# Kernel optimization log

Hardware: AMD Instinct MI355X
Metric: run time of the kernel (lower is better)

The kernel has to match this reference:

```python
import jax, jax.numpy as jnp
import numpy as np

N_NODES = 100000
IN_DIM = 64
OUT_DIM = 64
N_EDGES = 1600000


def _undirected_self_loops(edge_index, num_nodes):
    """Symmetrize, add self loops, coalesce (dedup+sort) like the torch module.
    edge_index is an integer constant, so we preprocess with numpy (no grads flow here).
    Returns (src, dst, w) where w are symmetric GCN normalization weights.
    """
    ei = np.asarray(edge_index, dtype=np.int64)
    loops = np.arange(num_nodes, dtype=np.int64)
    full_src = np.concatenate([ei[0], ei[1], loops])
    full_dst = np.concatenate([ei[1], ei[0], loops])
    keys = np.unique(full_src * num_nodes + full_dst)  # coalesce, sorted
    src = keys // num_nodes
    dst = keys % num_nodes
    deg = np.bincount(dst, minlength=num_nodes).clip(min=1)
    inv_sqrt = deg.astype(np.float32) ** -0.5
    w = inv_sqrt[src] * inv_sqrt[dst]
    return src, dst, w


def setup_inputs() -> dict:
    key = jax.random.key(0)
    kx, kw, kb, ke = jax.random.split(key, 4)
    x = jax.random.normal(kx, (N_NODES, IN_DIM), dtype=jnp.float32)
    # nn.Linear params: W (out, in), b (out,)
    W = jax.random.normal(kw, (OUT_DIM, IN_DIM), dtype=jnp.float32) / np.sqrt(IN_DIM)
    b = jax.random.normal(kb, (OUT_DIM,), dtype=jnp.float32) * 0.01
    edge_index = jax.random.randint(ke, (2, N_EDGES), 0, N_NODES, dtype=jnp.int64)
    return {"x": x, "edge_index": edge_index, "W": W, "b": b}


def reference(x, edge_index, W, b) -> jnp.ndarray:
    n = x.shape[0]
    src_np, dst_np, w_np = _undirected_self_loops(edge_index, n)
    src = jnp.asarray(src_np)
    dst = jnp.asarray(dst_np)
    w = jnp.asarray(w_np).astype(x.dtype)  # (E',)
    h = x @ W.T + b                         # (N, out_dim)
    msg = h[src] * w[:, None]               # gather + per-edge scale, (E', out_dim)
    out = jnp.zeros_like(h).at[dst].add(msg)  # scatter-add aggregation
    return out
```

## Files before the change

kernel.cpp:

```cpp
#include <hip/hip_runtime.h>
#include <hip/hip_bf16.h>
#include <stdint.h>

#define NN 100000
#define EE 1600000
#define CAP 128
#define NB 782
#define CAPB 5120
#define HTS 8192
#define EMPTY 0xFFFFFFFFu
#define GLIN 1563
#define GBIN 391

__device__ __forceinline__ unsigned int mix32(unsigned int x){
  x ^= x >> 16; x *= 0x7feb352du;
  x ^= x >> 15; x *= 0x846ca68bu;
  x ^= x >> 16;
  return x;
}

extern "C" __global__ __launch_bounds__(256)
void k_prep(const float* __restrict__ x, const float* __restrict__ W,
            const float* __restrict__ bias, __hip_bfloat16* __restrict__ hb,
            const int* __restrict__ ei, int* __restrict__ bcnt,
            unsigned int* __restrict__ bbuf){
  __shared__ __align__(16) char sm[25088];
  const int tid = threadIdx.x;
  const int bid = blockIdx.x;
  const bool isbin = (bid < GBIN);
  const int sub = isbin ? bid : (bid - GBIN);

  if (!isbin){
    float (*wt)[64]           = reinterpret_cast<float(*)[64]>(sm);
    __hip_bfloat16 (*xs)[68]  = reinterpret_cast<__hip_bfloat16(*)[68]>(sm + 16384);
    const int lane = tid & 63;
    const int wv   = tid >> 6;
    #pragma unroll
    for (int r = 0; r < 16; ++r){
      int i = r*4 + wv;
      wt[i][lane] = W[lane*64 + i];
    }
    const int nbase = sub * 64;
    #pragma unroll
    for (int r = 0; r < 4; ++r){
      int idx = r*256 + tid;
      int nl  = idx >> 4;
      int c4  = idx & 15;
      int n   = nbase + nl;
      float4 v = make_float4(0.f,0.f,0.f,0.f);
      if (n < NN) v = reinterpret_cast<const float4*>(x)[(size_t)n*16 + c4];
      xs[c4*4+0][nl] = __float2bfloat16(v.x);
      xs[c4*4+1][nl] = __float2bfloat16(v.y);
      xs[c4*4+2][nl] = __float2bfloat16(v.z);
      xs[c4*4+3][nl] = __float2bfloat16(v.w);
    }
    __syncthreads();

    const int og  = tid & 7;
    const int nl0 = (tid >> 3) * 2;
    float acc[2][8];
    #pragma unroll
    for (int t=0;t<2;++t){
      #pragma unroll
      for (int j=0;j<8;++j) acc[t][j]=0.f;
    }
    #pragma unroll 4
    for (int i=0;i<64;++i){
      float4 wa = *reinterpret_cast<const float4*>(&wt[i][og*8]);
      float4 wb = *reinterpret_cast<const float4*>(&wt[i][og*8+4]);
      unsigned xv = *reinterpret_cast<const unsigned*>(&xs[i][nl0]);
      float x0 = __uint_as_float(xv << 16);
      float x1 = __uint_as_float(xv & 0xFFFF0000u);
      acc[0][0] += x0*wa.x; acc[0][1] += x0*wa.y; acc[0][2] += x0*wa.z; acc[0][3] += x0*wa.w;
      acc[0][4] += x0*wb.x; acc[0][5] += x0*wb.y; acc[0][6] += x0*wb.z; acc[0][7] += x0*wb.w;
      acc[1][0] += x1*wa.x; acc[1][1] += x1*wa.y; acc[1][2] += x1*wa.z; acc[1][3] += x1*wa.w;
      acc[1][4] += x1*wb.x; acc[1][5] += x1*wb.y; acc[1][6] += x1*wb.z; acc[1][7] += x1*wb.w;
    }
    float4 b0 = reinterpret_cast<const float4*>(bias)[og*2];
    float4 b1 = reinterpret_cast<const float4*>(bias)[og*2+1];
    float bb[8] = {b0.x,b0.y,b0.z,b0.w,b1.x,b1.y,b1.z,b1.w};
    #pragma unroll
    for (int t=0;t<2;++t){
      int n = nbase + nl0 + t;
      if (n < NN){
        union { uint4 u4; __hip_bfloat16 v[8]; } pk;
        #pragma unroll
        for (int j=0;j<8;++j) pk.v[j] = __float2bfloat16(acc[t][j] + bb[j]);
        reinterpret_cast<uint4*>(&hb[(size_t)n*64])[og] = pk.u4;
      }
    }
  } else {
    int* hist  = reinterpret_cast<int*>(sm);
    int* bbase = hist + NB;
    int* bcur  = bbase + NB;
    for (int i = tid; i < NB; i += 256) hist[i] = 0;
    __syncthreads();
    const int e0 = sub * 4096;
    int ra[16], rc[16];
    #pragma unroll
    for (int r = 0; r < 16; ++r){
      int i = e0 + r*256 + tid;
      if (i < EE){
        ra[r] = ei[i]; rc[r] = ei[EE + i];
        atomicAdd(&hist[rc[r] >> 7], 1);
        atomicAdd(&hist[ra[r] >> 7], 1);
      } else ra[r] = -1;
    }
    __syncthreads();
    for (int bk = tid; bk < NB; bk += 256){
      int hh = hist[bk];
      bbase[bk] = hh ? atomicAdd(&bcnt[bk], hh) : 0;
      bcur[bk]  = 0;
    }
    __syncthreads();
    #pragma unroll
    for (int r = 0; r < 16; ++r){
      if (ra[r] >= 0){
        int a = ra[r], c = rc[r];
        int b1 = c >> 7, b2 = a >> 7;
        int p1 = bbase[b1] + atomicAdd(&bcur[b1], 1);
        int p2 = bbase[b2] + atomicAdd(&bcur[b2], 1);
        if (p1 < CAPB) bbuf[(size_t)b1*CAPB + p1] = ((unsigned)a << 7) | (unsigned)(c & 127);
        if (p2 < CAPB) bbuf[(size_t)b2*CAPB + p2] = ((unsigned)c << 7) | (unsigned)(a & 127);
      }
    }
  }
}

extern "C" __global__ __launch_bounds__(256)
void k_dedup(const int* __restrict__ bcnt, const unsigned int* __restrict__ bbuf,
             unsigned int* __restrict__ srclist, int* __restrict__ cnt,
             float* __restrict__ inv){
  __shared__ unsigned int HT[HTS];
  __shared__ int dcur[128];
  const int tid = threadIdx.x;
  const int b   = blockIdx.x;
  const int d0  = b << 7;
  uint4* HT4 = reinterpret_cast<uint4*>(HT);
  #pragma unroll
  for (int r = 0; r < 8; ++r) HT4[r*256 + tid] = make_uint4(EMPTY,EMPTY,EMPTY,EMPTY);
  if (tid < 128) dcur[tid] = 0;
  __syncthreads();

  int n = bcnt[b]; if (n > CAPB) n = CAPB;
  const unsigned int* buf = bbuf + (size_t)b * CAPB;
  for (int k = tid; k < n; k += 256){
    unsigned int pk  = buf[k];
    unsigned int idx = mix32(pk) & (HTS-1);
    for (;;){
      unsigned int prev = atomicCAS(&HT[idx], EMPTY, pk);
      if (prev == EMPTY || prev == pk) break;
      idx = (idx + 1) & (HTS-1);
    }
  }
  if (tid < 128 && d0 + tid < NN){
    unsigned int pk  = ((unsigned)(d0 + tid) << 7) | (unsigned)tid;
    unsigned int idx = mix32(pk) & (HTS-1);
    for (;;){
      unsigned int prev = atomicCAS(&HT[idx], EMPTY, pk);
      if (prev == EMPTY || prev == pk) break;
      idx = (idx + 1) & (HTS-1);
    }
  }
  __syncthreads();

  for (int i = tid; i < HTS; i += 256){
    unsigned int v = HT[i];
    if (v != EMPTY){
      int dl  = v & 127;
      int pos = atomicAdd(&dcur[dl], 1);
      if (pos < CAP) srclist[(size_t)(d0 + dl) * CAP + pos] = v >> 7;
    }
  }
  __syncthreads();
  if (tid < 128 && d0 + tid < NN){
    int c = dcur[tid];
    cnt[d0 + tid] = c;
    inv[d0 + tid] = rsqrtf((float)c);
  }
}

extern "C" __global__ __launch_bounds__(256)
void k_agg(const __hip_bfloat16* __restrict__ hb, const float* __restrict__ inv,
           const int* __restrict__ cnt, const unsigned int* __restrict__ srclist,
           float* __restrict__ out){
  __shared__ uint2 sv[4][CAP];
  const int wv   = threadIdx.x >> 6;
  const int lane = threadIdx.x & 63;
  const int g    = lane >> 4;
  const int pl   = lane & 15;
  const int d    = blockIdx.x*4 + wv;
  if (d >= NN) return;
  const unsigned int* reg = srclist + (size_t)d * CAP;
  int c = cnt[d]; if (c > CAP) c = CAP;
  const int cp = (c + 15) & ~15;

  if (lane < c){
    unsigned s = reg[lane];
    sv[wv][lane] = make_uint2(s, __float_as_uint(inv[s]));
  }
  if (64 + lane < c){
    unsigned s = reg[64 + lane];
    sv[wv][64 + lane] = make_uint2(s, __float_as_uint(inv[s]));
  }
  { int p = c + lane; if (p < cp) sv[wv][p] = make_uint2(0u, 0u); }

  const char* hbase = (const char*)hb;
  const int   boff  = pl << 3;
  float4 acc[4];
  #pragma unroll
  for (int u=0;u<4;++u) acc[u] = make_float4(0.f,0.f,0.f,0.f);
  #pragma unroll 1
  for (int j = 0; j < cp; j += 16){
    #pragma unroll
    for (int u = 0; u < 4; ++u){
      uint2 e = sv[wv][j + 4*u + g];
      float w = __uint_as_float(e.y);
      uint2 hv = *reinterpret_cast<const uint2*>(hbase + ((size_t)e.x << 7) + boff);
      acc[u].x += w * __uint_as_float(hv.x << 16);
      acc[u].y += w * __uint_as_float(hv.x & 0xFFFF0000u);
      acc[u].z += w * __uint_as_float(hv.y << 16);
      acc[u].w += w * __uint_as_float(hv.y & 0xFFFF0000u);
    }
  }
  float4 r;
  r.x = (acc[0].x+acc[1].x)+(acc[2].x+acc[3].x);
  r.y = (acc[0].y+acc[1].y)+(acc[2].y+acc[3].y);
  r.z = (acc[0].z+acc[1].z)+(acc[2].z+acc[3].z);
  r.w = (acc[0].w+acc[1].w)+(acc[2].w+acc[3].w);
  r.x += __shfl_xor(r.x, 16); r.y += __shfl_xor(r.y, 16);
  r.z += __shfl_xor(r.z, 16); r.w += __shfl_xor(r.w, 16);
  r.x += __shfl_xor(r.x, 32); r.y += __shfl_xor(r.y, 32);
  r.z += __shfl_xor(r.z, 32); r.w += __shfl_xor(r.w, 32);
  if (g == 0){
    float iv = inv[d];
    float4 o = make_float4(r.x*iv, r.y*iv, r.z*iv, r.w*iv);
    reinterpret_cast<float4*>(&out[(size_t)d*64])[pl] = o;
  }
}

extern "C" void kernel_launch(void* const* d_in, const int* in_sizes, int n_in,
                              void* d_out, int out_size, void* d_ws, size_t ws_size,
                              hipStream_t stream){
  (void)in_sizes; (void)n_in; (void)out_size; (void)ws_size;
  const float* x  = (const float*)d_in[0];
  const int*   ei = (const int*)  d_in[1];
  const float* W  = (const float*)d_in[2];
  const float* b  = (const float*)d_in[3];
  float* out = (float*)d_out;

  char* ws = (char*)d_ws;
  __hip_bfloat16* hb      = (__hip_bfloat16*)ws;
  float*          inv     = (float*)(ws + 12800000);
  int*            cnt     = (int*)  (ws + 13200000);
  unsigned int*   srclist = (unsigned int*)(ws + 13600000);
  int*            bcnt    = (int*)  (ws + 64800000);
  unsigned int*   bbuf    = (unsigned int*)(ws + 64804096);

  hipMemsetAsync(bcnt, 0, NB * 4, stream);

  k_prep  <<<GLIN + GBIN, 256, 0, stream>>>(x, W, b, hb, ei, bcnt, bbuf);
  k_dedup <<<NB, 256, 0, stream>>>(bcnt, bbuf, srclist, cnt, inv);
  k_agg   <<<(NN + 3)/4, 256, 0, stream>>>(hb, inv, cnt, srclist, out);
}
```

Measured before the change: 147.1 us.

## Single-pass edge binning, bf16 weights in LDS, nontemporal agg loads/stores

The binning blocks now process 2048 edges each using vectorized int4 loads. They reserve local slots with one atomic pass, packing both offsets into a register, instead of building a histogram and then running a second atomic pass. The linear blocks keep W as bf16 in LDS to shrink shared memory and allow higher occupancy. The aggregation kernel uses nontemporal loads for source lists and nontemporal stores for the output, and unrolls the gather loop by two. Risks: the 16-bit packed local offsets assume per-bucket counts stay small, and the bf16 weights add rounding error.

```diff
diff --git a/kernel.cpp b/kernel.cpp
--- a/kernel.cpp
+++ b/kernel.cpp
@@ -9,8 +9,11 @@
 #define CAPB 5120
 #define HTS 8192
 #define EMPTY 0xFFFFFFFFu
+#define BCHUNK 2048
+#define GBIN 782
 #define GLIN 1563
-#define GBIN 391
+
+typedef float  fx4 __attribute__((ext_vector_type(4)));
 
 __device__ __forceinline__ unsigned int mix32(unsigned int x){
   x ^= x >> 16; x *= 0x7feb352du;
@@ -24,21 +27,21 @@
             const float* __restrict__ bias, __hip_bfloat16* __restrict__ hb,
             const int* __restrict__ ei, int* __restrict__ bcnt,
             unsigned int* __restrict__ bbuf){
-  __shared__ __align__(16) char sm[25088];
+  __shared__ __align__(16) char sm[17920];
   const int tid = threadIdx.x;
   const int bid = blockIdx.x;
   const bool isbin = (bid < GBIN);
   const int sub = isbin ? bid : (bid - GBIN);
 
   if (!isbin){
-    float (*wt)[64]           = reinterpret_cast<float(*)[64]>(sm);
-    __hip_bfloat16 (*xs)[68]  = reinterpret_cast<__hip_bfloat16(*)[68]>(sm + 16384);
+    __hip_bfloat16 (*wt)[72] = reinterpret_cast<__hip_bfloat16(*)[72]>(sm);
+    __hip_bfloat16 (*xs)[68] = reinterpret_cast<__hip_bfloat16(*)[68]>(sm + 9216);
     const int lane = tid & 63;
     const int wv   = tid >> 6;
     #pragma unroll
     for (int r = 0; r < 16; ++r){
       int i = r*4 + wv;
-      wt[i][lane] = W[lane*64 + i];
+      wt[i][lane] = __float2bfloat16(W[lane*64 + i]);
     }
     const int nbase = sub * 64;
     #pragma unroll
@@ -66,15 +69,18 @@
     }
     #pragma unroll 4
     for (int i=0;i<64;++i){
-      float4 wa = *reinterpret_cast<const float4*>(&wt[i][og*8]);
-      float4 wb = *reinterpret_cast<const float4*>(&wt[i][og*8+4]);
+      uint4 wq = *reinterpret_cast<const uint4*>(&wt[i][og*8]);
+      float w0 = __uint_as_float(wq.x << 16), w1 = __uint_as_float(wq.x & 0xFFFF0000u);
+      float w2 = __uint_as_float(wq.y << 16), w3 = __uint_as_float(wq.y & 0xFFFF0000u);
+      float w4 = __uint_as_float(wq.z << 16), w5 = __uint_as_float(wq.z & 0xFFFF0000u);
+      float w6 = __uint_as_float(wq.w << 16), w7 = __uint_as_float(wq.w & 0xFFFF0000u);
       unsigned xv = *reinterpret_cast<const unsigned*>(&xs[i][nl0]);
       float x0 = __uint_as_float(xv << 16);
       float x1 = __uint_as_float(xv & 0xFFFF0000u);
-      acc[0][0] += x0*wa.x; acc[0][1] += x0*wa.y; acc[0][2] += x0*wa.z; acc[0][3] += x0*wa.w;
-      acc[0][4] += x0*wb.x; acc[0][5] += x0*wb.y; acc[0][6] += x0*wb.z; acc[0][7] += x0*wb.w;
-      acc[1][0] += x1*wa.x; acc[1][1] += x1*wa.y; acc[1][2] += x1*wa.z; acc[1][3] += x1*wa.w;
-      acc[1][4] += x1*wb.x; acc[1][5] += x1*wb.y; acc[1][6] += x1*wb.z; acc[1][7] += x1*wb.w;
+      acc[0][0] += x0*w0; acc[0][1] += x0*w1; acc[0][2] += x0*w2; acc[0][3] += x0*w3;
+      acc[0][4] += x0*w4; acc[0][5] += x0*w5; acc[0][6] += x0*w6; acc[0][7] += x0*w7;
+      acc[1][0] += x1*w0; acc[1][1] += x1*w1; acc[1][2] += x1*w2; acc[1][3] += x1*w3;
+      acc[1][4] += x1*w4; acc[1][5] += x1*w5; acc[1][6] += x1*w6; acc[1][7] += x1*w7;
     }
     float4 b0 = reinterpret_cast<const float4*>(bias)[og*2];
     float4 b1 = reinterpret_cast<const float4*>(bias)[og*2+1];
@@ -90,40 +96,49 @@
       }
     }
   } else {
-    int* hist  = reinterpret_cast<int*>(sm);
-    int* bbase = hist + NB;
-    int* bcur  = bbase + NB;
-    for (int i = tid; i < NB; i += 256) hist[i] = 0;
-    __syncthreads();
-    const int e0 = sub * 4096;
-    int ra[16], rc[16];
-    #pragma unroll
-    for (int r = 0; r < 16; ++r){
-      int i = e0 + r*256 + tid;
-      if (i < EE){
-        ra[r] = ei[i]; rc[r] = ei[EE + i];
-        atomicAdd(&hist[rc[r] >> 7], 1);
-        atomicAdd(&hist[ra[r] >> 7], 1);
-      } else ra[r] = -1;
-    }
+    int* bcur  = reinterpret_cast<int*>(sm);
+    int* bbase = bcur + NB;
+    for (int i = tid; i < NB; i += 256) bcur[i] = 0;
+    __syncthreads();
+    const int e0 = sub * BCHUNK;
+    const int4* ea4 = reinterpret_cast<const int4*>(ei);
+    const int4* ec4 = reinterpret_cast<const int4*>(ei + EE);
+    int4 A0, C0, A1, C1;
+    unsigned P[8];
+    {
+      int idx0 = (e0 >> 2) + tid;
+      int idx1 = idx0 + 256;
+      if (idx0*4 < EE){ A0 = ea4[idx0]; C0 = ec4[idx0]; }
+      else { A0 = make_int4(-1,-1,-1,-1); C0 = A0; }
+      if (idx1*4 < EE){ A1 = ea4[idx1]; C1 = ec4[idx1]; }
+      else { A1 = make_int4(-1,-1,-1,-1); C1 = A1; }
+    }
+#define RESV(a,c,slot) \
+    if ((a) >= 0){ \
+      unsigned p1 = (unsigned)atomicAdd(&bcur[(c) >> 7], 1); \
+      unsigned p2 = (unsigned)atomicAdd(&bcur[(a) >> 7], 1); \
+      P[slot] = p1 | (p2 << 16); \
+    }
+    RESV(A0.x, C0.x, 0) RESV(A0.y, C0.y, 1) RESV(A0.z, C0.z, 2) RESV(A0.w, C0.w, 3)
+    RESV(A1.x, C1.x, 4) RESV(A1.y, C1.y, 5) RESV(A1.z, C1.z, 6) RESV(A1.w, C1.w, 7)
+#undef RESV
     __syncthreads();
     for (int bk = tid; bk < NB; bk += 256){
-      int hh = hist[bk];
+      int hh = bcur[bk];
       bbase[bk] = hh ? atomicAdd(&bcnt[bk], hh) : 0;
-      bcur[bk]  = 0;
-    }
-    __syncthreads();
-    #pragma unroll
-    for (int r = 0; r < 16; ++r){
-      if (ra[r] >= 0){
-        int a = ra[r], c = rc[r];
-        int b1 = c >> 7, b2 = a >> 7;
-        int p1 = bbase[b1] + atomicAdd(&bcur[b1], 1);
-        int p2 = bbase[b2] + atomicAdd(&bcur[b2], 1);
-        if (p1 < CAPB) bbuf[(size_t)b1*CAPB + p1] = ((unsigned)a << 7) | (unsigned)(c & 127);
-        if (p2 < CAPB) bbuf[(size_t)b2*CAPB + p2] = ((unsigned)c << 7) | (unsigned)(a & 127);
-      }
-    }
+    }
+    __syncthreads();
+#define PLACE(a,c,slot) \
+    if ((a) >= 0){ \
+      int b1 = (c) >> 7, b2 = (a) >> 7; \
+      unsigned q1 = (unsigned)bbase[b1] + (P[slot] & 0xFFFFu); \
+      unsigned q2 = (unsigned)bbase[b2] + (P[slot] >> 16); \
+      if (q1 < CAPB) bbuf[(size_t)b1*CAPB + q1] = ((unsigned)(a) << 7) | (unsigned)((c) & 127); \
+      if (q2 < CAPB) bbuf[(size_t)b2*CAPB + q2] = ((unsigned)(c) << 7) | (unsigned)((a) & 127); \
+    }
+    PLACE(A0.x, C0.x, 0) PLACE(A0.y, C0.y, 1) PLACE(A0.z, C0.z, 2) PLACE(A0.w, C0.w, 3)
+    PLACE(A1.x, C1.x, 4) PLACE(A1.y, C1.y, 5) PLACE(A1.z, C1.z, 6) PLACE(A1.w, C1.w, 7)
+#undef PLACE
   }
 }
 
@@ -196,11 +211,11 @@
   const int cp = (c + 15) & ~15;
 
   if (lane < c){
-    unsigned s = reg[lane];
+    unsigned s = __builtin_nontemporal_load(reg + lane);
     sv[wv][lane] = make_uint2(s, __float_as_uint(inv[s]));
   }
   if (64 + lane < c){
-    unsigned s = reg[64 + lane];
+    unsigned s = __builtin_nontemporal_load(reg + 64 + lane);
     sv[wv][64 + lane] = make_uint2(s, __float_as_uint(inv[s]));
   }
   { int p = c + lane; if (p < cp) sv[wv][p] = make_uint2(0u, 0u); }
@@ -210,7 +225,7 @@
   float4 acc[4];
   #pragma unroll
   for (int u=0;u<4;++u) acc[u] = make_float4(0.f,0.f,0.f,0.f);
-  #pragma unroll 1
+  #pragma unroll 2
   for (int j = 0; j < cp; j += 16){
     #pragma unroll
     for (int u = 0; u < 4; ++u){
@@ -234,8 +249,8 @@
   r.z += __shfl_xor(r.z, 32); r.w += __shfl_xor(r.w, 32);
   if (g == 0){
     float iv = inv[d];
-    float4 o = make_float4(r.x*iv, r.y*iv, r.z*iv, r.w*iv);
-    reinterpret_cast<float4*>(&out[(size_t)d*64])[pl] = o;
+    fx4 o; o.x = r.x*iv; o.y = r.y*iv; o.z = r.z*iv; o.w = r.w*iv;
+    __builtin_nontemporal_store(o, reinterpret_cast<fx4*>(&out[(size_t)d*64]) + pl);
   }
 }
 
@@ -257,9 +272,9 @@
   int*            bcnt    = (int*)  (ws + 64800000);
   unsigned int*   bbuf    = (unsigned int*)(ws + 64804096);
 
-  hipMemsetAsync(bcnt, 0, NB * 4, stream);
-
-  k_prep  <<<GLIN + GBIN, 256, 0, stream>>>(x, W, b, hb, ei, bcnt, bbuf);
+  (void)hipMemsetAsync(bcnt, 0, NB * 4, stream);
+
+  k_prep  <<<GBIN + GLIN, 256, 0, stream>>>(x, W, b, hb, ei, bcnt, bbuf);
   k_dedup <<<NB, 256, 0, stream>>>(bcnt, bbuf, srclist, cnt, inv);
   k_agg   <<<(NN + 3)/4, 256, 0, stream>>>(hb, inv, cnt, srclist, out);
 }
```

Result: slower. 162.6 us (+10.6%).
